# Optimization experiments

Measured on AMD Instinct MI355X. Metric: run time of the kernel, lower is better.

The kernel has to match this reference:

```python
import jax, jax.numpy as jnp
import numpy as np
import math

NUM_HEADS = 8


def setup_inputs() -> dict:
    key = jax.random.key(0)
    ks = jax.random.split(key, 6)
    b, s, e = 4, 2048, 512
    x = jax.random.normal(ks[0], (b, s, e), dtype=jnp.float32)
    # 0/1 adjacency matrix as float (it multiplies the scores in the module)
    adj = jax.random.randint(ks[1], (b, s, s), 0, 2).astype(jnp.float32)
    scale = 0.02
    Wqkv_w = jax.random.normal(ks[2], (3 * e, e), dtype=jnp.float32) * scale
    Wqkv_b = jax.random.normal(ks[3], (3 * e,), dtype=jnp.float32) * scale
    out_w = jax.random.normal(ks[4], (e, e), dtype=jnp.float32) * scale
    out_b = jax.random.normal(ks[5], (e,), dtype=jnp.float32) * scale
    return {"x": x, "adj": adj, "Wqkv_w": Wqkv_w, "Wqkv_b": Wqkv_b,
            "out_w": out_w, "out_b": out_b}


def reference(x, adj, Wqkv_w, Wqkv_b, out_w, out_b):
    b, s, e = x.shape
    h = NUM_HEADS
    d = e // h
    # fused qkv projection: (b, s, 3*e) -> (b, s, 3, h, d)
    qkv = (x @ Wqkv_w.T + Wqkv_b).reshape(b, s, 3, h, d)
    qkv = jnp.transpose(qkv, (2, 0, 3, 1, 4))  # (3, b, h, s, d)
    q, k, v = qkv[0], qkv[1], qkv[2]
    inv_sqrt_d = 1.0 / math.sqrt(d)
    scores = jnp.einsum('bhqd,bhkd->bhqk', q, k) * inv_sqrt_d
    scores = jnp.clip(scores * adj[:, None, :, :], -10000.0, 10000.0)
    attn = jax.nn.softmax(scores, axis=-1)
    out = jnp.einsum('bhqk,bhkd->bhqd', attn, v)
    out = jnp.transpose(out, (0, 2, 1, 3)).reshape(b, s, e)  # (b, s, h*d)
    return out @ out_w.T + out_b
```

## Files before the change

### kernel.cpp

```cpp
#include <hip/hip_runtime.h>


typedef __attribute__((ext_vector_type(8))) short bf16x8;
typedef __attribute__((ext_vector_type(4))) float f32x4;
typedef __attribute__((ext_vector_type(4))) unsigned short ushort4v;
typedef __attribute__((ext_vector_type(4))) _Float16 f16x4;
typedef __attribute__((ext_vector_type(8))) _Float16 f16x8;
typedef __attribute__((ext_vector_type(2))) __fp16 h16x2;
typedef __attribute__((ext_vector_type(2))) unsigned long long u64x2;

#if __has_builtin(__builtin_amdgcn_exp2f)
#define EXP2F(x) __builtin_amdgcn_exp2f(x)
#else
#define EXP2F(x) exp2f(x)
#endif

#define QSCALE 0.18033688011112042f

__device__ __forceinline__ unsigned short f2bf(float f) {
  unsigned int u = __float_as_uint(f);
  u += 0x7FFFu + ((u >> 16) & 1u);
  return (unsigned short)(u >> 16);
}
__device__ __forceinline__ unsigned short f2h(float f) {
  union { _Float16 h; unsigned short u; } cv;
  cv.h = (_Float16)f;
  return cv.u;
}

__device__ __forceinline__ int sbit(unsigned w, int pos) {
  return ((int)(w << (31 - pos))) >> 31;
}

__device__ __forceinline__ f16x8 pk8(const float* p) {
  union { struct { h16x2 a, b, c, d; } s; f16x8 v; } u;
  u.s.a = __builtin_amdgcn_cvt_pkrtz(p[0], p[1]);
  u.s.b = __builtin_amdgcn_cvt_pkrtz(p[2], p[3]);
  u.s.c = __builtin_amdgcn_cvt_pkrtz(p[4], p[5]);
  u.s.d = __builtin_amdgcn_cvt_pkrtz(p[6], p[7]);
  return u.v;
}

__device__ __forceinline__ f32x4 mfma_pv(f16x8 a, f16x8 b, f32x4 c) {
#if __has_builtin(__builtin_amdgcn_mfma_f32_16x16x32_f16)
  return __builtin_amdgcn_mfma_f32_16x16x32_f16(a, b, c, 0, 0, 0);
#else
  union { f16x8 v; struct { f16x4 lo, hi; } s; } ua, ub;
  ua.v = a; ub.v = b;
  c = __builtin_amdgcn_mfma_f32_16x16x16f16(ua.s.lo, ub.s.lo, c, 0, 0, 0);
  return __builtin_amdgcn_mfma_f32_16x16x16f16(ua.s.hi, ub.s.hi, c, 0, 0, 0);
#endif
}

__global__ __launch_bounds__(256) void prep_k(const float* __restrict__ x,
                                              unsigned short* __restrict__ x_bf,
                                              const float* __restrict__ wqkv,
                                              unsigned short* __restrict__ wqkv_bf,
                                              const float* __restrict__ outw,
                                              unsigned short* __restrict__ outw_bf,
                                              const float* __restrict__ adj,
                                              unsigned long long* __restrict__ abits) {
  const int bid = blockIdx.x;
  if (bid < 5120) {
    const float* in; unsigned short* out; int i;
    if (bid < 4096) { in = x; out = x_bf; i = bid * 256 + threadIdx.x; }
    else if (bid < 4864) { in = wqkv; out = wqkv_bf; i = (bid - 4096) * 256 + threadIdx.x; }
    else { in = outw; out = outw_bf; i = (bid - 4864) * 256 + threadIdx.x; }
    float4 v = ((const float4*)in)[i];
    ushort4v o;
    o[0] = f2bf(v.x); o[1] = f2bf(v.y); o[2] = f2bf(v.z); o[3] = f2bf(v.w);
    ((ushort4v*)out)[i] = o;
  } else {
    const int gw = (bid - 5120) * 4 + (threadIdx.x >> 6);
    const int l = threadIdx.x & 63;
    const int b = gw >> 11, q = gw & 2047;
    const float4* row = (const float4*)(adj + ((size_t)b * 2048 + q) * 2048) + l;
    unsigned long long* ob = abits + ((size_t)b * 8 * 2048 + q) * 4;
#pragma unroll
    for (int it = 0; it < 8; ++it) {
      const float4 v = row[(size_t)it * 64];
      const unsigned long long w0 = __ballot(v.x != 0.f);
      const unsigned long long w1 = __ballot(v.y != 0.f);
      const unsigned long long w2 = __ballot(v.z != 0.f);
      const unsigned long long w3 = __ballot(v.w != 0.f);
      if (l == 0) {
        ob[(size_t)it * 8192 + 0] = w0;
        ob[(size_t)it * 8192 + 1] = w1;
        ob[(size_t)it * 8192 + 2] = w2;
        ob[(size_t)it * 8192 + 3] = w3;
      }
    }
  }
}

__global__ __launch_bounds__(256, 3) void gemm128_k(const unsigned short* __restrict__ A,
                                                    const unsigned short* __restrict__ Bt,
                                                    const float* __restrict__ bias, int Kdim,
                                                    int Ntiles, unsigned short* __restrict__ q_out,
                                                    unsigned short* __restrict__ k_out,
                                                    unsigned short* __restrict__ v_out) {
  __shared__ union {
    struct { unsigned short A[2][128][40], B[2][128][40]; } s;
    unsigned short T[64][136];
  } u;

  const int t = threadIdx.x;
  const int lane = t & 63, w = t >> 6, ln = lane & 15, quad = lane >> 4;
  const int xcd = blockIdx.x & 7, loc = blockIdx.x >> 3;
  const int mt = xcd * ((gridDim.x >> 3) / Ntiles) + loc / Ntiles;
  const int nt = loc % Ntiles;
  const int wm = (w >> 1) * 64, wn = (w & 1) * 64;
  const int strow = t >> 2, stcol = (t & 3) * 8;

  const size_t abase = (size_t)(mt * 128 + strow) * Kdim + stcol;
  const size_t bbase = (size_t)(nt * 128 + strow) * Kdim + stcol;

  f32x4 acc[4][4];
#pragma unroll
  for (int i = 0; i < 4; ++i)
#pragma unroll
    for (int j = 0; j < 4; ++j) acc[i][j] = (f32x4){0.f, 0.f, 0.f, 0.f};

  bf16x8 a0 = *(const bf16x8*)(A + abase);
  bf16x8 a1 = *(const bf16x8*)(A + abase + (size_t)64 * Kdim);
  bf16x8 b0 = *(const bf16x8*)(Bt + bbase);
  bf16x8 b1 = *(const bf16x8*)(Bt + bbase + (size_t)64 * Kdim);
  *(bf16x8*)&u.s.A[0][strow][stcol] = a0;
  *(bf16x8*)&u.s.A[0][64 + strow][stcol] = a1;
  *(bf16x8*)&u.s.B[0][strow][stcol] = b0;
  *(bf16x8*)&u.s.B[0][64 + strow][stcol] = b1;
  __syncthreads();

  const int iters = Kdim >> 5;
  for (int it = 0; it < iters; ++it) {
    const int cur = it & 1, nxt = cur ^ 1;

    const int kn = ((it + 1) << 5) & (Kdim - 1);
    a0 = *(const bf16x8*)(A + abase + kn);
    a1 = *(const bf16x8*)(A + abase + (size_t)64 * Kdim + kn);
    b0 = *(const bf16x8*)(Bt + bbase + kn);
    b1 = *(const bf16x8*)(Bt + bbase + (size_t)64 * Kdim + kn);

    bf16x8 bfr[4];
#pragma unroll
    for (int nf = 0; nf < 4; ++nf)
      bfr[nf] = *(const bf16x8*)&u.s.B[cur][wn + nf * 16 + ln][quad * 8];
#pragma unroll
    for (int mf = 0; mf < 4; ++mf) {
      bf16x8 af = *(const bf16x8*)&u.s.A[cur][wm + mf * 16 + ln][quad * 8];
#pragma unroll
      for (int nf = 0; nf < 4; ++nf)
        acc[mf][nf] = __builtin_amdgcn_mfma_f32_16x16x32_bf16(af, bfr[nf], acc[mf][nf], 0, 0, 0);
    }

    if (it + 1 < iters) {
      *(bf16x8*)&u.s.A[nxt][strow][stcol] = a0;
      *(bf16x8*)&u.s.A[nxt][64 + strow][stcol] = a1;
      *(bf16x8*)&u.s.B[nxt][strow][stcol] = b0;
      *(bf16x8*)&u.s.B[nxt][64 + strow][stcol] = b1;
      __syncthreads();
    }
  }

  if (nt >= 8) {
    const int bb = mt >> 4, sq0 = (mt & 15) * 128;
#pragma unroll
    for (int half = 0; half < 2; ++half) {
      __syncthreads();
      if ((w & 1) == half) {
#pragma unroll
        for (int nf = 0; nf < 4; ++nf) {
          const float bv = bias[nt * 128 + half * 64 + nf * 16 + ln];
#pragma unroll
          for (int mf = 0; mf < 4; ++mf)
#pragma unroll
            for (int r = 0; r < 4; ++r)
              u.T[nf * 16 + ln][wm + mf * 16 + quad * 4 + r] = f2h(acc[mf][nf][r] + bv);
        }
      }
      __syncthreads();
#pragma unroll
      for (int rep = 0; rep < 4; ++rep) {
        const int row = rep * 16 + (t >> 4), c = t & 15;
        const bf16x8 val = *(const bf16x8*)&u.T[row][c * 8];
        const int hd = (nt - 8) * 128 + half * 64 + row;
        const int hh = hd >> 6, dd = hd & 63;
        *(bf16x8*)(v_out + ((size_t)(bb * 8 + hh) * 64 + dd) * 2048 + sq0 + c * 8) = val;
      }
    }
    return;
  }

#pragma unroll
  for (int mf = 0; mf < 4; ++mf) {
    const int m = mt * 128 + wm + mf * 16 + quad * 4;
#pragma unroll
    for (int nf = 0; nf < 4; ++nf) {
      const int n = nt * 128 + wn + nf * 16 + ln;
      const float bv = bias[n];
      const int hd = n & 511;
      const int hh = hd >> 6, dd = hd & 63;
      const int bb = m >> 11, sq = m & 2047;
      if (n < 512) {
#pragma unroll
        for (int r = 0; r < 4; ++r)
          q_out[((size_t)(bb * 8 + hh) * 2048 + sq + r) * 64 + dd] =
              f2bf((acc[mf][nf][r] + bv) * QSCALE);
      } else {
#pragma unroll
        for (int r = 0; r < 4; ++r)
          k_out[((size_t)(bb * 8 + hh) * 2048 + sq + r) * 64 + dd] = f2bf(acc[mf][nf][r] + bv);
      }
    }
  }
}

__global__ __launch_bounds__(256, 3) void gemm64_k(const unsigned short* __restrict__ A,
                                                   const unsigned short* __restrict__ Bt,
                                                   const float* __restrict__ bias,
                                                   float* __restrict__ f_out) {
  __shared__ struct { unsigned short A[2][128][40], B[2][64][40]; } s;

  const int t = threadIdx.x;
  const int lane = t & 63, w = t >> 6, ln = lane & 15, quad = lane >> 4;
  const int xcd = blockIdx.x & 7, loc = blockIdx.x >> 3;
  const int mt = xcd * 8 + (loc >> 3);
  const int nt = loc & 7;
  const int wm = (w >> 1) * 64, wn = (w & 1) * 32;
  const int strow = t >> 2, stcol = (t & 3) * 8;

  const size_t abase = (size_t)(mt * 128 + strow) * 512 + stcol;
  const size_t bbase = (size_t)(nt * 64 + strow) * 512 + stcol;

  f32x4 acc[4][2];
#pragma unroll
  for (int i = 0; i < 4; ++i)
#pragma unroll
    for (int j = 0; j < 2; ++j) acc[i][j] = (f32x4){0.f, 0.f, 0.f, 0.f};

  bf16x8 a0 = *(const bf16x8*)(A + abase);
  bf16x8 a1 = *(const bf16x8*)(A + abase + (size_t)64 * 512);
  bf16x8 b0 = *(const bf16x8*)(Bt + bbase);
  *(bf16x8*)&s.A[0][strow][stcol] = a0;
  *(bf16x8*)&s.A[0][64 + strow][stcol] = a1;
  *(bf16x8*)&s.B[0][strow][stcol] = b0;
  __syncthreads();

  for (int it = 0; it < 16; ++it) {
    const int cur = it & 1, nxt = cur ^ 1;

    const int kn = ((it + 1) << 5) & 511;
    a0 = *(const bf16x8*)(A + abase + kn);
    a1 = *(const bf16x8*)(A + abase + (size_t)64 * 512 + kn);
    b0 = *(const bf16x8*)(Bt + bbase + kn);

    bf16x8 bfr[2];
#pragma unroll
    for (int nf = 0; nf < 2; ++nf)
      bfr[nf] = *(const bf16x8*)&s.B[cur][wn + nf * 16 + ln][quad * 8];
#pragma unroll
    for (int mf = 0; mf < 4; ++mf) {
      bf16x8 af = *(const bf16x8*)&s.A[cur][wm + mf * 16 + ln][quad * 8];
#pragma unroll
      for (int nf = 0; nf < 2; ++nf)
        acc[mf][nf] = __builtin_amdgcn_mfma_f32_16x16x32_bf16(af, bfr[nf], acc[mf][nf], 0, 0, 0);
    }

    if (it + 1 < 16) {
      *(bf16x8*)&s.A[nxt][strow][stcol] = a0;
      *(bf16x8*)&s.A[nxt][64 + strow][stcol] = a1;
      *(bf16x8*)&s.B[nxt][strow][stcol] = b0;
      __syncthreads();
    }
  }

#pragma unroll
  for (int mf = 0; mf < 4; ++mf) {
    const int m = mt * 128 + wm + mf * 16 + quad * 4;
#pragma unroll
    for (int nf = 0; nf < 2; ++nf) {
      const int n = nt * 64 + wn + nf * 16 + ln;
      const float bv = bias[n];
#pragma unroll
      for (int r = 0; r < 4; ++r) f_out[(size_t)(m + r) * 512 + n] = acc[mf][nf][r] + bv;
    }
  }
}

__global__ __launch_bounds__(256, 2) void attn_k(const unsigned short* __restrict__ Qg,
                                                 const unsigned short* __restrict__ Kg,
                                                 const unsigned short* __restrict__ Vg,
                                                 const unsigned long long* __restrict__ Mg,
                                                 unsigned short* __restrict__ Og) {
  __shared__ unsigned short K_lds[2][64][64];
  __shared__ unsigned short V_lds[2][64][64];

  const int t = threadIdx.x;
  const int w = t >> 6, lane = t & 63, ln = lane & 15, quad = lane >> 4;
  const int bh = blockIdx.x & 31, qt = blockIdx.x >> 5, bb = bh >> 3;
  const int sbase = qt * 128;

  const unsigned short* Qp = Qg + (size_t)bh * (2048 * 64);
  const unsigned short* Kp = Kg + (size_t)bh * (2048 * 64);
  const unsigned short* Vp = Vg + (size_t)bh * (64 * 2048);
  const unsigned long long* Mb = Mg + ((size_t)bb * 8 * 2048 + sbase + w * 32 + ln) * 4;

  bf16x8 qf[2][2];
#pragma unroll
  for (int qg = 0; qg < 2; ++qg) {
    const int qrow = sbase + w * 32 + qg * 16 + ln;
    qf[qg][0] = *(const bf16x8*)(Qp + (size_t)qrow * 64 + quad * 8);
    qf[qg][1] = *(const bf16x8*)(Qp + (size_t)qrow * 64 + 32 + quad * 8);
  }

  const _Float16 one_h = (_Float16)((ln == 0) ? 1.0f : 0.0f);
  const f16x8 vf_one = (f16x8){one_h, one_h, one_h, one_h, one_h, one_h, one_h, one_h};

  const f32x4 zf = (f32x4){0.f, 0.f, 0.f, 0.f};

  f32x4 acc_o[2][4];
#pragma unroll
  for (int qg = 0; qg < 2; ++qg)
#pragma unroll
    for (int dg = 0; dg < 4; ++dg) acc_o[qg][dg] = zf;
  f32x4 acc_1[2] = {zf, zf};

  const int strow = t >> 2;
  const int stcol = (t & 3) * 16;
  const int c0 = (t & 3) * 2;
  const int gkw = (strow & 3) | (((strow >> 3) & 1) << 2);
  const int gvw = strow & 7;

  const unsigned short* Kl = Kp + (size_t)strow * 64 + stcol;
  const unsigned short* Vl = Vp + (size_t)strow * 2048 + stcol;

  bf16x8 kr0 = *(const bf16x8*)(Kl);
  bf16x8 kr1 = *(const bf16x8*)(Kl + 8);
  bf16x8 vr0 = *(const bf16x8*)(Vl);
  bf16x8 vr1 = *(const bf16x8*)(Vl + 8);
  *(bf16x8*)&K_lds[0][strow][(c0 ^ gkw) << 3] = kr0;
  *(bf16x8*)&K_lds[0][strow][((c0 + 1) ^ gkw) << 3] = kr1;
  *(bf16x8*)&V_lds[0][strow][(c0 ^ gvw) << 3] = vr0;
  *(bf16x8*)&V_lds[0][strow][((c0 + 1) ^ gvw) << 3] = vr1;
  u64x2 Wlo[2], Whi[2];
#pragma unroll
  for (int qg = 0; qg < 2; ++qg) {
    Wlo[qg] = *(const u64x2*)(Mb + qg * 64);
    Whi[qg] = *(const u64x2*)(Mb + qg * 64 + 2);
  }
  __syncthreads();

  const int kperm = ((ln >> 2) << 3) + (ln & 3);
  const int gkr = (ln & 3) | (((ln >> 2) & 1) << 2);
  const int gvr = ln & 7;
  const int kc = (quad ^ gkr) << 3;
  const unsigned q2 = quad << 1;

  for (int kts = 0; kts < 8; ++kts) {
    const size_t itn = (size_t)((kts < 7) ? kts + 1 : 0) * 8192;
    u64x2 nWlo[2], nWhi[2];
#pragma unroll
    for (int qg = 0; qg < 2; ++qg) {
      nWlo[qg] = *(const u64x2*)(Mb + itn + qg * 64);
      nWhi[qg] = *(const u64x2*)(Mb + itn + qg * 64 + 2);
    }

#pragma unroll
    for (int j = 0; j < 4; ++j) {
      const int kt = kts * 4 + j;
      const int cur = j & 1, nxt = cur ^ 1;

      kr0 = *(const bf16x8*)(Kl + (size_t)(kt + 1) * 4096);
      kr1 = *(const bf16x8*)(Kl + (size_t)(kt + 1) * 4096 + 8);
      vr0 = *(const bf16x8*)(Vl + (kt + 1) * 64);
      vr1 = *(const bf16x8*)(Vl + (kt + 1) * 64 + 8);

      f32x4 sc[2][4];
      __builtin_amdgcn_s_setprio(1);
#pragma unroll
      for (int h = 0; h < 2; ++h)
#pragma unroll
        for (int e = 0; e < 2; ++e) {
          const int krow = h * 32 + kperm + e * 4;
          bf16x8 kf0 = *(const bf16x8*)&K_lds[cur][krow][kc];
          bf16x8 kf1 = *(const bf16x8*)&K_lds[cur][krow][kc ^ 32];
#pragma unroll
          for (int qg = 0; qg < 2; ++qg) {
            f32x4 z = __builtin_amdgcn_mfma_f32_16x16x32_bf16(kf0, qf[qg][0], zf, 0, 0, 0);
            sc[qg][h * 2 + e] = __builtin_amdgcn_mfma_f32_16x16x32_bf16(kf1, qf[qg][1], z, 0, 0, 0);
          }
        }
      __builtin_amdgcn_s_setprio(0);

      f16x8 vfa[2][4];
#pragma unroll
      for (int h = 0; h < 2; ++h)
#pragma unroll
        for (int dg = 0; dg < 4; ++dg)
          vfa[h][dg] = *(const f16x8*)&V_lds[cur][dg * 16 + ln][((h * 4 + quad) ^ gvr) << 3];

      f16x8 pa[2][2];
#pragma unroll
      for (int qg = 0; qg < 2; ++qg) {
        const unsigned s0 = (unsigned)(Wlo[qg][0] >> (j >= 2 ? 32 : 0)) >> q2;
        const unsigned s1 = (unsigned)(Wlo[qg][1] >> (j >= 2 ? 32 : 0)) >> q2;
        const unsigned s2 = (unsigned)(Whi[qg][0] >> (j >= 2 ? 32 : 0)) >> q2;
        const unsigned s3 = (unsigned)(Whi[qg][1] >> (j >= 2 ? 32 : 0)) >> q2;
#pragma unroll
        for (int h = 0; h < 2; ++h) {
          float p[8];
#pragma unroll
          for (int e = 0; e < 2; ++e) {
            const int pos = (j & 1) * 16 + h * 8 + e;
            p[e * 4 + 0] =
                EXP2F(__int_as_float(__float_as_int(sc[qg][h * 2 + e][0]) & sbit(s0, pos)));
            p[e * 4 + 1] =
                EXP2F(__int_as_float(__float_as_int(sc[qg][h * 2 + e][1]) & sbit(s1, pos)));
            p[e * 4 + 2] =
                EXP2F(__int_as_float(__float_as_int(sc[qg][h * 2 + e][2]) & sbit(s2, pos)));
            p[e * 4 + 3] =
                EXP2F(__int_as_float(__float_as_int(sc[qg][h * 2 + e][3]) & sbit(s3, pos)));
          }
          pa[qg][h] = pk8(p);
        }
      }

      __builtin_amdgcn_s_setprio(1);
#pragma unroll
      for (int h = 0; h < 2; ++h)
#pragma unroll
        for (int qg = 0; qg < 2; ++qg) {
#pragma unroll
          for (int dg = 0; dg < 4; ++dg)
            acc_o[qg][dg] = mfma_pv(pa[qg][h], vfa[h][dg], acc_o[qg][dg]);
          acc_1[qg] = mfma_pv(pa[qg][h], vf_one, acc_1[qg]);
        }
      __builtin_amdgcn_s_setprio(0);

      if (kt < 31) {
        *(bf16x8*)&K_lds[nxt][strow][(c0 ^ gkw) << 3] = kr0;
        *(bf16x8*)&K_lds[nxt][strow][((c0 + 1) ^ gkw) << 3] = kr1;
        *(bf16x8*)&V_lds[nxt][strow][(c0 ^ gvw) << 3] = vr0;
        *(bf16x8*)&V_lds[nxt][strow][((c0 + 1) ^ gvw) << 3] = vr1;
        __syncthreads();
      }
    }
    Wlo[0] = nWlo[0]; Wlo[1] = nWlo[1];
    Whi[0] = nWhi[0]; Whi[1] = nWhi[1];
  }

  unsigned short* Op = Og + (size_t)bb * 2048 * 512 + (size_t)(bh & 7) * 64;
#pragma unroll
  for (int qg = 0; qg < 2; ++qg)
#pragma unroll
    for (int r = 0; r < 4; ++r) {
      const float inv = 1.0f / __shfl(acc_1[qg][r], quad * 16);
      const int sq = sbase + w * 32 + qg * 16 + quad * 4 + r;
#pragma unroll
      for (int dg = 0; dg < 4; ++dg)
        Op[(size_t)sq * 512 + dg * 16 + ln] = f2bf(acc_o[qg][dg][r] * inv);
    }
}

extern "C" void kernel_launch(void* const* d_in, const int* in_sizes, int n_in, void* d_out,
                              int out_size, void* d_ws, size_t ws_size, hipStream_t stream) {
  const float* x = (const float*)d_in[0];
  const float* adj = (const float*)d_in[1];
  const float* wqkv = (const float*)d_in[2];
  const float* bqkv = (const float*)d_in[3];
  const float* outw = (const float*)d_in[4];
  const float* outb = (const float*)d_in[5];
  float* out = (float*)d_out;

  char* ws = (char*)d_ws;
  unsigned short* x_bf = (unsigned short*)(ws);
  unsigned short* wqkv_bf = (unsigned short*)(ws + 8388608);
  unsigned short* outw_bf = (unsigned short*)(ws + 9961472);
  unsigned long long* abits = (unsigned long long*)(ws + 10485760);
  unsigned short* Qb = (unsigned short*)(ws + 27262976);
  unsigned short* Kb = (unsigned short*)(ws + 35651584);
  unsigned short* Vb = (unsigned short*)(ws + 44040192);
  unsigned short* Ob = (unsigned short*)(ws + 52428800);

  prep_k<<<7168, 256, 0, stream>>>(x, x_bf, wqkv, wqkv_bf, outw, outw_bf, adj, abits);

  gemm128_k<<<768, 256, 0, stream>>>(x_bf, wqkv_bf, bqkv, 512, 12, Qb, Kb, Vb);

  attn_k<<<512, 256, 0, stream>>>(Qb, Kb, Vb, abits, Ob);

  gemm64_k<<<512, 256, 0, stream>>>(Ob, outw_bf, outb, out);
}
```

Measured before the change: 199.2 us.

## Stage two K/V tiles per barrier with four-slot LDS ring in attention

The attention kernel now stages two 64-key K/V tiles at a time into a four-slot LDS ring instead of one tile into a double buffer. This halves the number of __syncthreads barriers and gives global loads two tiles of compute to hide behind. In exchange LDS use doubles to 64 KB per block and more registers hold in-flight prefetches. That may cut occupancy from the intended 2 blocks per CU.

```diff
diff --git a/kernel.cpp b/kernel.cpp
--- a/kernel.cpp
+++ b/kernel.cpp
@@ -292,8 +292,8 @@
                                                  const unsigned short* __restrict__ Vg,
                                                  const unsigned long long* __restrict__ Mg,
                                                  unsigned short* __restrict__ Og) {
-  __shared__ unsigned short K_lds[2][64][64];
-  __shared__ unsigned short V_lds[2][64][64];
+  __shared__ unsigned short K_lds[4][64][64];
+  __shared__ unsigned short V_lds[4][64][64];
 
   const int t = threadIdx.x;
   const int w = t >> 6, lane = t & 63, ln = lane & 15, quad = lane >> 4;
@@ -334,14 +334,26 @@
   const unsigned short* Kl = Kp + (size_t)strow * 64 + stcol;
   const unsigned short* Vl = Vp + (size_t)strow * 2048 + stcol;
 
-  bf16x8 kr0 = *(const bf16x8*)(Kl);
-  bf16x8 kr1 = *(const bf16x8*)(Kl + 8);
-  bf16x8 vr0 = *(const bf16x8*)(Vl);
-  bf16x8 vr1 = *(const bf16x8*)(Vl + 8);
-  *(bf16x8*)&K_lds[0][strow][(c0 ^ gkw) << 3] = kr0;
-  *(bf16x8*)&K_lds[0][strow][((c0 + 1) ^ gkw) << 3] = kr1;
-  *(bf16x8*)&V_lds[0][strow][(c0 ^ gvw) << 3] = vr0;
-  *(bf16x8*)&V_lds[0][strow][((c0 + 1) ^ gvw) << 3] = vr1;
+#define STAGE(B, K0, K1, V0, V1)                               \
+  {                                                            \
+    *(bf16x8*)&K_lds[B][strow][(c0 ^ gkw) << 3] = K0;          \
+    *(bf16x8*)&K_lds[B][strow][((c0 + 1) ^ gkw) << 3] = K1;    \
+    *(bf16x8*)&V_lds[B][strow][(c0 ^ gvw) << 3] = V0;          \
+    *(bf16x8*)&V_lds[B][strow][((c0 + 1) ^ gvw) << 3] = V1;    \
+  }
+
+  {
+    bf16x8 k00 = *(const bf16x8*)(Kl);
+    bf16x8 k01 = *(const bf16x8*)(Kl + 8);
+    bf16x8 v00 = *(const bf16x8*)(Vl);
+    bf16x8 v01 = *(const bf16x8*)(Vl + 8);
+    bf16x8 k10 = *(const bf16x8*)(Kl + 4096);
+    bf16x8 k11 = *(const bf16x8*)(Kl + 4096 + 8);
+    bf16x8 v10 = *(const bf16x8*)(Vl + 64);
+    bf16x8 v11 = *(const bf16x8*)(Vl + 64 + 8);
+    STAGE(0, k00, k01, v00, v01);
+    STAGE(1, k10, k11, v10, v11);
+  }
   u64x2 Wlo[2], Whi[2];
 #pragma unroll
   for (int qg = 0; qg < 2; ++qg) {
@@ -356,7 +368,60 @@
   const int kc = (quad ^ gkr) << 3;
   const unsigned q2 = quad << 1;
 
+#define COMP(J)                                                                          \
+  {                                                                                      \
+    f32x4 sc[2][4];                                                                      \
+    __builtin_amdgcn_s_setprio(1);                                                       \
+    _Pragma("unroll") for (int h = 0; h < 2; ++h)                                        \
+        _Pragma("unroll") for (int e = 0; e < 2; ++e) {                                  \
+      const int krow = h * 32 + kperm + e * 4;                                           \
+      bf16x8 kf0 = *(const bf16x8*)&K_lds[J][krow][kc];                                  \
+      bf16x8 kf1 = *(const bf16x8*)&K_lds[J][krow][kc ^ 32];                             \
+      _Pragma("unroll") for (int qg = 0; qg < 2; ++qg) {                                 \
+        f32x4 z = __builtin_amdgcn_mfma_f32_16x16x32_bf16(kf0, qf[qg][0], zf, 0, 0, 0);  \
+        sc[qg][h * 2 + e] =                                                              \
+            __builtin_amdgcn_mfma_f32_16x16x32_bf16(kf1, qf[qg][1], z, 0, 0, 0);         \
+      }                                                                                  \
+    }                                                                                    \
+    __builtin_amdgcn_s_setprio(0);                                                       \
+    f16x8 vfa[2][4];                                                                     \
+    _Pragma("unroll") for (int h = 0; h < 2; ++h)                                        \
+        _Pragma("unroll") for (int dg = 0; dg < 4; ++dg) vfa[h][dg] =                    \
+            *(const f16x8*)&V_lds[J][dg * 16 + ln][((h * 4 + quad) ^ gvr) << 3];         \
+    f16x8 pa[2][2];                                                                      \
+    _Pragma("unroll") for (int qg = 0; qg < 2; ++qg) {                                   \
+      const unsigned s0 = (unsigned)(Wlo[qg][0] >> ((J) >= 2 ? 32 : 0)) >> q2;           \
+      const unsigned s1 = (unsigned)(Wlo[qg][1] >> ((J) >= 2 ? 32 : 0)) >> q2;           \
+      const unsigned s2 = (unsigned)(Whi[qg][0] >> ((J) >= 2 ? 32 : 0)) >> q2;           \
+      const unsigned s3 = (unsigned)(Whi[qg][1] >> ((J) >= 2 ? 32 : 0)) >> q2;           \
+      _Pragma("unroll") for (int h = 0; h < 2; ++h) {                                    \
+        float p[8];                                                                      \
+        _Pragma("unroll") for (int e = 0; e < 2; ++e) {                                  \
+          const int pos = ((J)&1) * 16 + h * 8 + e;                                      \
+          p[e * 4 + 0] =                                                                 \
+              EXP2F(__int_as_float(__float_as_int(sc[qg][h * 2 + e][0]) & sbit(s0, pos))); \
+          p[e * 4 + 1] =                                                                 \
+              EXP2F(__int_as_float(__float_as_int(sc[qg][h * 2 + e][1]) & sbit(s1, pos))); \
+          p[e * 4 + 2] =                                                                 \
+              EXP2F(__int_as_float(__float_as_int(sc[qg][h * 2 + e][2]) & sbit(s2, pos))); \
+          p[e * 4 + 3] =                                                                 \
+              EXP2F(__int_as_float(__float_as_int(sc[qg][h * 2 + e][3]) & sbit(s3, pos))); \
+        }                                                                                \
+        pa[qg][h] = pk8(p);                                                              \
+      }                                                                                  \
+    }                                                                                    \
+    __builtin_amdgcn_s_setprio(1);                                                       \
+    _Pragma("unroll") for (int h = 0; h < 2; ++h)                                        \
+        _Pragma("unroll") for (int qg = 0; qg < 2; ++qg) {                               \
+      _Pragma("unroll") for (int dg = 0; dg < 4; ++dg) acc_o[qg][dg] =                   \
+          mfma_pv(pa[qg][h], vfa[h][dg], acc_o[qg][dg]);                                 \
+      acc_1[qg] = mfma_pv(pa[qg][h], vf_one, acc_1[qg]);                                 \
+    }                                                                                    \
+    __builtin_amdgcn_s_setprio(0);                                                       \
+  }
+
   for (int kts = 0; kts < 8; ++kts) {
+    const int b4 = kts * 4;
     const size_t itn = (size_t)((kts < 7) ? kts + 1 : 0) * 8192;
     u64x2 nWlo[2], nWhi[2];
 #pragma unroll
@@ -365,89 +430,52 @@
       nWhi[qg] = *(const u64x2*)(Mb + itn + qg * 64 + 2);
     }
 
-#pragma unroll
-    for (int j = 0; j < 4; ++j) {
-      const int kt = kts * 4 + j;
-      const int cur = j & 1, nxt = cur ^ 1;
-
-      kr0 = *(const bf16x8*)(Kl + (size_t)(kt + 1) * 4096);
-      kr1 = *(const bf16x8*)(Kl + (size_t)(kt + 1) * 4096 + 8);
-      vr0 = *(const bf16x8*)(Vl + (kt + 1) * 64);
-      vr1 = *(const bf16x8*)(Vl + (kt + 1) * 64 + 8);
-
-      f32x4 sc[2][4];
-      __builtin_amdgcn_s_setprio(1);
-#pragma unroll
-      for (int h = 0; h < 2; ++h)
-#pragma unroll
-        for (int e = 0; e < 2; ++e) {
-          const int krow = h * 32 + kperm + e * 4;
-          bf16x8 kf0 = *(const bf16x8*)&K_lds[cur][krow][kc];
-          bf16x8 kf1 = *(const bf16x8*)&K_lds[cur][krow][kc ^ 32];
-#pragma unroll
-          for (int qg = 0; qg < 2; ++qg) {
-            f32x4 z = __builtin_amdgcn_mfma_f32_16x16x32_bf16(kf0, qf[qg][0], zf, 0, 0, 0);
-            sc[qg][h * 2 + e] = __builtin_amdgcn_mfma_f32_16x16x32_bf16(kf1, qf[qg][1], z, 0, 0, 0);
-          }
-        }
-      __builtin_amdgcn_s_setprio(0);
-
-      f16x8 vfa[2][4];
-#pragma unroll
-      for (int h = 0; h < 2; ++h)
-#pragma unroll
-        for (int dg = 0; dg < 4; ++dg)
-          vfa[h][dg] = *(const f16x8*)&V_lds[cur][dg * 16 + ln][((h * 4 + quad) ^ gvr) << 3];
-
-      f16x8 pa[2][2];
-#pragma unroll
-      for (int qg = 0; qg < 2; ++qg) {
-        const unsigned s0 = (unsigned)(Wlo[qg][0] >> (j >= 2 ? 32 : 0)) >> q2;
-        const unsigned s1 = (unsigned)(Wlo[qg][1] >> (j >= 2 ? 32 : 0)) >> q2;
-        const unsigned s2 = (unsigned)(Whi[qg][0] >> (j >= 2 ? 32 : 0)) >> q2;
-        const unsigned s3 = (unsigned)(Whi[qg][1] >> (j >= 2 ? 32 : 0)) >> q2;
-#pragma unroll
-        for (int h = 0; h < 2; ++h) {
-          float p[8];
-#pragma unroll
-          for (int e = 0; e < 2; ++e) {
-            const int pos = (j & 1) * 16 + h * 8 + e;
-            p[e * 4 + 0] =
-                EXP2F(__int_as_float(__float_as_int(sc[qg][h * 2 + e][0]) & sbit(s0, pos)));
-            p[e * 4 + 1] =
-                EXP2F(__int_as_float(__float_as_int(sc[qg][h * 2 + e][1]) & sbit(s1, pos)));
-            p[e * 4 + 2] =
-                EXP2F(__int_as_float(__float_as_int(sc[qg][h * 2 + e][2]) & sbit(s2, pos)));
-            p[e * 4 + 3] =
-                EXP2F(__int_as_float(__float_as_int(sc[qg][h * 2 + e][3]) & sbit(s3, pos)));
-          }
-          pa[qg][h] = pk8(p);
-        }
+    {
+      bf16x8 k20 = *(const bf16x8*)(Kl + (size_t)(b4 + 2) * 4096);
+      bf16x8 k21 = *(const bf16x8*)(Kl + (size_t)(b4 + 2) * 4096 + 8);
+      bf16x8 v20 = *(const bf16x8*)(Vl + (b4 + 2) * 64);
+      bf16x8 v21 = *(const bf16x8*)(Vl + (b4 + 2) * 64 + 8);
+      bf16x8 k30 = *(const bf16x8*)(Kl + (size_t)(b4 + 3) * 4096);
+      bf16x8 k31 = *(const bf16x8*)(Kl + (size_t)(b4 + 3) * 4096 + 8);
+      bf16x8 v30 = *(const bf16x8*)(Vl + (b4 + 3) * 64);
+      bf16x8 v31 = *(const bf16x8*)(Vl + (b4 + 3) * 64 + 8);
+
+      COMP(0);
+      COMP(1);
+
+      STAGE(2, k20, k21, v20, v21);
+      STAGE(3, k30, k31, v30, v31);
+      __syncthreads();
+    }
+
+    {
+      bf16x8 k40, k41, v40, v41, k50, k51, v50, v51;
+      if (kts < 7) {
+        k40 = *(const bf16x8*)(Kl + (size_t)(b4 + 4) * 4096);
+        k41 = *(const bf16x8*)(Kl + (size_t)(b4 + 4) * 4096 + 8);
+        v40 = *(const bf16x8*)(Vl + (b4 + 4) * 64);
+        v41 = *(const bf16x8*)(Vl + (b4 + 4) * 64 + 8);
+        k50 = *(const bf16x8*)(Kl + (size_t)(b4 + 5) * 4096);
+        k51 = *(const bf16x8*)(Kl + (size_t)(b4 + 5) * 4096 + 8);
+        v50 = *(const bf16x8*)(Vl + (b4 + 5) * 64);
+        v51 = *(const bf16x8*)(Vl + (b4 + 5) * 64 + 8);
       }
 
-      __builtin_amdgcn_s_setprio(1);
-#pragma unroll
-      for (int h = 0; h < 2; ++h)
-#pragma unroll
-        for (int qg = 0; qg < 2; ++qg) {
-#pragma unroll
-          for (int dg = 0; dg < 4; ++dg)
-            acc_o[qg][dg] = mfma_pv(pa[qg][h], vfa[h][dg], acc_o[qg][dg]);
-          acc_1[qg] = mfma_pv(pa[qg][h], vf_one, acc_1[qg]);
-        }
-      __builtin_amdgcn_s_setprio(0);
-
-      if (kt < 31) {
-        *(bf16x8*)&K_lds[nxt][strow][(c0 ^ gkw) << 3] = kr0;
-        *(bf16x8*)&K_lds[nxt][strow][((c0 + 1) ^ gkw) << 3] = kr1;
-        *(bf16x8*)&V_lds[nxt][strow][(c0 ^ gvw) << 3] = vr0;
-        *(bf16x8*)&V_lds[nxt][strow][((c0 + 1) ^ gvw) << 3] = vr1;
+      COMP(2);
+      COMP(3);
+
+      if (kts < 7) {
+        STAGE(0, k40, k41, v40, v41);
+        STAGE(1, k50, k51, v50, v51);
         __syncthreads();
       }
     }
+
     Wlo[0] = nWlo[0]; Wlo[1] = nWlo[1];
     Whi[0] = nWhi[0]; Whi[1] = nWhi[1];
   }
+#undef COMP
+#undef STAGE
 
   unsigned short* Op = Og + (size_t)bb * 2048 * 512 + (size_t)(bh & 7) * 64;
 #pragma unroll
```

Result: slower. 205.5 us (+3.1%).
